# Kernel tuning notes

Hardware: AMD Instinct MI355X
Metric: run time of the kernel (lower is better)

Reference implementation:

```python
import jax, jax.numpy as jnp
import numpy as np

EMB = 1024
HID = 4096
B = 2
T = 4096
NUM_BLOCK = 24
EPS = 1e-6


def rmsnorm(x):
    # unparameterized RMS normalization over last dim
    return x * jax.lax.rsqrt(jnp.mean(jnp.square(x), axis=-1, keepdims=True) + EPS)


def setup_inputs() -> dict:
    key = jax.random.key(0)
    k1, k2, k3, k4 = jax.random.split(key, 4)
    x = jax.random.normal(k1, (B, T, EMB), dtype=jnp.float32)
    W1 = 0.02 * jax.random.normal(k2, (HID, EMB), dtype=jnp.float32)
    W2 = 0.02 * jax.random.normal(k3, (HID, EMB), dtype=jnp.float32)
    W3 = (0.02 / np.sqrt(NUM_BLOCK)) * jax.random.normal(k4, (EMB, HID), dtype=jnp.float32)
    return {"x": x, "W1": W1, "W2": W2, "W3": W3}


def bar_quadratic_causal_preact_stable(a, b):
    # y_t = (1/t^2) * sum_{i<=t} sum_{j<=t} exp(a_i + b_j), per feature channel.
    # exp factorizes, so compute stably via log-cumsum-exp along the seq axis.
    seq = a.shape[1]
    log_t = jnp.log(jnp.arange(1, seq + 1, dtype=a.dtype))  # [T]
    la = jax.lax.cumlogsumexp(a, axis=1)  # [B,T,H]
    lb = jax.lax.cumlogsumexp(b, axis=1)  # [B,T,H]
    return jnp.exp(la + lb - 2.0 * log_t[None, :, None])


def reference(x, W1, W2, W3):
    r = rmsnorm(x)
    a = jnp.einsum('bte,he->bth', r, W1)  # fc_1, no bias
    b = jnp.einsum('bte,he->bth', r, W2)  # fc_2, no bias
    r = bar_quadratic_causal_preact_stable(a, b)
    r = rmsnorm(r)
    r = jnp.einsum('bth,eh->bte', r, W3)  # fc_3, no bias
    return x + r
```

## Files before the change

### kernel.cpp

```cpp
#include <hip/hip_runtime.h>
#include <hip/hip_fp8.h>

#define EMB 1024
#define HID 4096
#define NB 2
#define TT 4096
#define MROWS (NB*TT)
#define N1 (2*HID)
#define CHUNK 128
#define NCH 32

typedef short short8 __attribute__((ext_vector_type(8)));
typedef float v4f   __attribute__((ext_vector_type(4)));

__device__ __forceinline__ unsigned short f2bf(float f) {
  unsigned int u = __float_as_uint(f);
  u += 0x7FFFu + ((u >> 16) & 1u);
  return (unsigned short)(u >> 16);
}
__device__ __forceinline__ float bf2f(unsigned short s) {
  return __uint_as_float(((unsigned int)s) << 16);
}
__device__ __forceinline__ float h2f(unsigned short u) {
  return (float)(*(const _Float16*)&u);
}
__device__ __forceinline__ unsigned char f2e4m3(float f) {
  __hip_fp8_e4m3 q(f);
  return *(unsigned char*)&q;
}
__device__ __forceinline__ float e4m32f(unsigned char c) {
  __hip_fp8_e4m3 q = *(__hip_fp8_e4m3*)&c;
  return (float)q;
}
__device__ __forceinline__ void g2l16(const void* g, void* l) {
  __builtin_amdgcn_global_load_lds(
      (const __attribute__((address_space(1))) void*)g,
      (__attribute__((address_space(3))) void*)l, 16, 0, 0);
}

__device__ __forceinline__ float block_reduce_sum(float v, float* sbuf) {
  #pragma unroll
  for (int off = 32; off; off >>= 1) v += __shfl_down(v, off, 64);
  int lane = threadIdx.x & 63, w = threadIdx.x >> 6;
  if (lane == 0) sbuf[w] = v;
  __syncthreads();
  return sbuf[0] + sbuf[1] + sbuf[2] + sbuf[3];
}

__global__ __launch_bounds__(256) void conv_all(const float* __restrict__ W1,
                                                const float* __restrict__ W2,
                                                const float* __restrict__ W3,
                                                unsigned short* __restrict__ o12,
                                                unsigned char* __restrict__ o3) {
  size_t i = ((size_t)blockIdx.x*256 + threadIdx.x)*4;
  if (i < 2ull*HID*EMB) {
    const float* s = (i < (size_t)HID*EMB) ? (W1 + i) : (W2 + (i - (size_t)HID*EMB));
    float4 v = *(const float4*)s;
    ushort4 u; u.x=f2bf(v.x); u.y=f2bf(v.y); u.z=f2bf(v.z); u.w=f2bf(v.w);
    *(ushort4*)(o12 + i) = u;
  } else {
    size_t off = i - 2ull*HID*EMB;
    float4 v = *(const float4*)(W3 + off);
    uchar4 u; u.x=f2e4m3(v.x*64.f); u.y=f2e4m3(v.y*64.f);
             u.z=f2e4m3(v.z*64.f); u.w=f2e4m3(v.w*64.f);
    *(uchar4*)(o3 + off) = u;
  }
}

__global__ __launch_bounds__(256) void rmsnorm_x(const float* __restrict__ x,
                                                 unsigned short* __restrict__ r) {
  __shared__ float sbuf[4];
  int row = blockIdx.x;
  float4 v = *(const float4*)(x + (size_t)row*EMB + threadIdx.x*4);
  float ss = v.x*v.x + v.y*v.y + v.z*v.z + v.w*v.w;
  float tot = block_reduce_sum(ss, sbuf);
  float sc = rsqrtf(tot * (1.0f/EMB) + 1e-6f);
  ushort4 o; o.x=f2bf(v.x*sc); o.y=f2bf(v.y*sc); o.z=f2bf(v.z*sc); o.w=f2bf(v.w*sc);
  *(ushort4*)(r + (size_t)row*EMB + threadIdx.x*4) = o;
}

__global__ __launch_bounds__(256) void normq(const unsigned short* __restrict__ y,
                                             unsigned char* __restrict__ y8) {
  __shared__ float sbuf[4];
  int row = blockIdx.x;
  const unsigned short* p = y + (size_t)row*HID + threadIdx.x*16;
  short8 v0 = *(const short8*)p;
  short8 v1 = *(const short8*)(p+8);
  float f[16]; float ss = 0.f;
  #pragma unroll
  for (int j=0;j<8;++j){ f[j]=bf2f((unsigned short)v0[j]); f[j+8]=bf2f((unsigned short)v1[j]); }
  #pragma unroll
  for (int j=0;j<16;++j) ss += f[j]*f[j];
  float tot = block_reduce_sum(ss, sbuf);
  float sc = rsqrtf(tot*(1.0f/HID) + 1e-6f);
  unsigned int w[4];
  #pragma unroll
  for (int g=0; g<4; ++g) {
    unsigned int a0 = f2e4m3(f[g*4+0]*sc);
    unsigned int a1 = f2e4m3(f[g*4+1]*sc);
    unsigned int a2 = f2e4m3(f[g*4+2]*sc);
    unsigned int a3 = f2e4m3(f[g*4+3]*sc);
    w[g] = a0 | (a1<<8) | (a2<<16) | (a3<<24);
  }
  uint4 o; o.x=w[0]; o.y=w[1]; o.z=w[2]; o.w=w[3];
  *(uint4*)(y8 + (size_t)row*HID + threadIdx.x*16) = o;
}

__global__ __launch_bounds__(512, 2)
void gemm_exp(const unsigned short* __restrict__ A,
              const unsigned short* __restrict__ Bt,
              unsigned char* __restrict__ C8,
              float* __restrict__ part,
              int K, int N) {
  __shared__ short lds[4][2][256*32];
  const int tid  = threadIdx.x;
  const int lane = tid & 63;
  const int wid  = tid >> 6;
  const int wr   = wid >> 2;
  const int wc   = wid & 3;
  const int bid  = blockIdx.x;
  const int s0   = bid >> 3;
  const int colTile = ((bid & 7) << 2) | (s0 & 3);
  const int rowTile = s0 >> 2;
  const int rowBase = rowTile << 8;
  const int colBase = colTile << 8;
  const int NT = K >> 5;

  v4f acc[8][4];
  #pragma unroll
  for (int i=0;i<8;++i)
    #pragma unroll
    for (int j=0;j<4;++j) acc[i][j] = (v4f){0.f,0.f,0.f,0.f};

  auto stage = [&](int t) {
    const int buf = t & 3;
    const int k0  = t << 5;
    #pragma unroll
    for (int j = 0; j < 2; ++j) {
      int slot = j*512 + tid;
      int msw  = slot >> 2;
      int m    = msw ^ ((msw >> 2) & 1);
      int c    = (slot & 3) ^ (m & 3);
      g2l16(A + (size_t)(rowBase + m)*K + k0 + c*8, &lds[buf][0][slot*8]);
    }
    #pragma unroll
    for (int j = 0; j < 2; ++j) {
      int slot = j*512 + tid;
      int msw  = slot >> 2;
      int m    = msw ^ ((msw >> 2) & 1);
      int c    = (slot & 3) ^ (m & 3);
      g2l16(Bt + (size_t)(colBase + m)*K + k0 + c*8, &lds[buf][1][slot*8]);
    }
  };

  stage(0);
  if (NT > 1) stage(1);

  const int q   = lane >> 4;
  const int r15 = lane & 15;

  for (int t = 0; t < NT; ++t) {
    if (t + 2 < NT) stage(t + 2);
    if (t + 2 < NT)      asm volatile("s_waitcnt vmcnt(8)" ::: "memory");
    else if (t + 1 < NT) asm volatile("s_waitcnt vmcnt(4)" ::: "memory");
    else                 asm volatile("s_waitcnt vmcnt(0)" ::: "memory");
    __builtin_amdgcn_s_barrier();
    __builtin_amdgcn_sched_barrier(0);

    const short* lA = &lds[t & 3][0][0];
    const short* lB = &lds[t & 3][1][0];
    short8 aF[4], bF[4], aG[4];
    #pragma unroll
    for (int mt = 0; mt < 4; ++mt) {
      int m = wr*128 + mt*16 + r15;
      int slot = ((m ^ ((m >> 2) & 1)) << 2) | (q ^ (m & 3));
      aF[mt] = *(const short8*)&lA[slot*8];
    }
    #pragma unroll
    for (int nt = 0; nt < 4; ++nt) {
      int n = wc*64 + nt*16 + r15;
      int slot = ((n ^ ((n >> 2) & 1)) << 2) | (q ^ (n & 3));
      bF[nt] = *(const short8*)&lB[slot*8];
    }
    #pragma unroll
    for (int mt = 0; mt < 4; ++mt) {
      int m = wr*128 + (mt+4)*16 + r15;
      int slot = ((m ^ ((m >> 2) & 1)) << 2) | (q ^ (m & 3));
      aG[mt] = *(const short8*)&lA[slot*8];
    }
    __builtin_amdgcn_s_setprio(1);
    #pragma unroll
    for (int mt = 0; mt < 4; ++mt)
      #pragma unroll
      for (int nt = 0; nt < 4; ++nt)
        acc[mt][nt] = __builtin_amdgcn_mfma_f32_16x16x32_bf16(aF[mt], bF[nt], acc[mt][nt], 0, 0, 0);
    #pragma unroll
    for (int mt = 0; mt < 4; ++mt)
      #pragma unroll
      for (int nt = 0; nt < 4; ++nt)
        acc[mt+4][nt] = __builtin_amdgcn_mfma_f32_16x16x32_bf16(aG[mt], bF[nt], acc[mt+4][nt], 0, 0, 0);
    __builtin_amdgcn_s_setprio(0);
  }

  float csum[4] = {0.f, 0.f, 0.f, 0.f};
  #pragma unroll
  for (int mt = 0; mt < 8; ++mt) {
    #pragma unroll
    for (int nt = 0; nt < 4; ++nt) {
      int col = colBase + wc*64 + nt*16 + r15;
      #pragma unroll
      for (int rr = 0; rr < 4; ++rr) {
        int row = rowBase + wr*128 + mt*16 + q*4 + rr;
        float e = __expf(acc[mt][nt][rr]);
        C8[(size_t)row*N + col] = f2e4m3(e);
        csum[nt] += e;
      }
    }
  }
  const int chunk = rowTile*2 + wr;
  #pragma unroll
  for (int nt = 0; nt < 4; ++nt) {
    float v = csum[nt];
    v += __shfl_xor(v, 16, 64);
    v += __shfl_xor(v, 32, 64);
    if (lane < 16)
      part[(size_t)(colBase + wc*64 + nt*16 + lane)*64 + chunk] = v;
  }
}

__global__ __launch_bounds__(256, 2)
void gemm_out(const unsigned char* __restrict__ A8,
              const unsigned char* __restrict__ B8,
              unsigned short* __restrict__ Ph,
              int K, int KCH, int N) {
  __shared__ unsigned char lA8[128*128];
  __shared__ unsigned char lB8[128*128];
  const int tid  = threadIdx.x;
  const int lane = tid & 63;
  const int wm   = (tid >> 6) >> 1, wn = (tid >> 6) & 1;
  const int rowBase = blockIdx.x * 128;
  const int colBase = blockIdx.y * 128;
  const int kStart  = blockIdx.z * KCH;

  v4f acc[4][4];
  #pragma unroll
  for (int i=0;i<4;++i)
    #pragma unroll
    for (int j=0;j<4;++j) acc[i][j] = (v4f){0.f,0.f,0.f,0.f};

  for (int k0 = kStart; k0 < kStart + KCH; k0 += 128) {
    #pragma unroll
    for (int j = 0; j < 4; ++j) {
      int s = j*256 + tid;
      int m = s >> 3;
      int c = (s & 7) ^ (m & 7);
      g2l16(A8 + (size_t)(rowBase + m)*K + k0 + c*16, &lA8[s*16]);
    }
    #pragma unroll
    for (int j = 0; j < 4; ++j) {
      int s = j*256 + tid;
      int m = s >> 3;
      int c = (s & 7) ^ (m & 7);
      g2l16(B8 + (size_t)(colBase + m)*K + k0 + c*16, &lB8[s*16]);
    }
    __syncthreads();
    #pragma unroll
    for (int s2 = 0; s2 < 4; ++s2) {
      const int quad = lane >> 4;
      const int cc = s2*2 + (quad >> 1);
      const int hh = quad & 1;
      long aF[4], bF[4];
      #pragma unroll
      for (int mt = 0; mt < 4; ++mt) {
        int ml = wm*64 + mt*16 + (lane & 15);
        aF[mt] = *(const long*)&lA8[ml*128 + ((cc ^ (ml & 7))<<4) + (hh<<3)];
      }
      #pragma unroll
      for (int nt = 0; nt < 4; ++nt) {
        int nl = wn*64 + nt*16 + (lane & 15);
        bF[nt] = *(const long*)&lB8[nl*128 + ((cc ^ (nl & 7))<<4) + (hh<<3)];
      }
      #pragma unroll
      for (int mt = 0; mt < 4; ++mt)
        #pragma unroll
        for (int nt = 0; nt < 4; ++nt)
          acc[mt][nt] = __builtin_amdgcn_mfma_f32_16x16x32_fp8_fp8(aF[mt], bF[nt], acc[mt][nt], 0, 0, 0);
    }
    __syncthreads();
  }

  const int quad = lane >> 4, c15 = lane & 15;
  #pragma unroll
  for (int mt = 0; mt < 4; ++mt) {
    #pragma unroll
    for (int nt = 0; nt < 4; ++nt) {
      int col = colBase + wn*64 + nt*16 + c15;
      #pragma unroll
      for (int r = 0; r < 4; ++r) {
        int row = rowBase + wm*64 + mt*16 + quad*4 + r;
        size_t idx = ((size_t)blockIdx.z*MROWS + row)*N + col;
        _Float16 h = (_Float16)acc[mt][nt][r];
        Ph[idx] = *(unsigned short*)&h;
      }
    }
  }
}

__global__ __launch_bounds__(256) void scan_prefix(float* __restrict__ part) {
  int idx = blockIdx.x*256 + threadIdx.x;
  int col = idx >> 1, bb = idx & 1;
  float* p = part + (size_t)col*64 + bb*NCH;
  float run = 0.f;
  #pragma unroll
  for (int c = 0; c < NCH; ++c) { float v = p[c]; p[c] = run; run += v; }
}

__global__ __launch_bounds__(256) void scan_emit(const unsigned char* __restrict__ ab,
                                                 const float* __restrict__ part,
                                                 unsigned short* __restrict__ y) {
  int h = blockIdx.x*256 + threadIdx.x;
  int cy = blockIdx.y, bb = blockIdx.z;
  float sa = part[(size_t)h*64 + bb*NCH + cy];
  float sb = part[(size_t)(HID + h)*64 + bb*NCH + cy];
  const unsigned char* pa = ab + ((size_t)(bb*TT + cy*CHUNK))*N1 + h;
  const unsigned char* pb = pa + HID;
  unsigned short* py = y + ((size_t)(bb*TT + cy*CHUNK))*HID + h;
  int t0 = cy*CHUNK;
  #pragma unroll 4
  for (int i = 0; i < CHUNK; ++i) {
    sa += e4m32f(pa[(size_t)i*N1]);
    sb += e4m32f(pb[(size_t)i*N1]);
    float inv = 1.0f / (float)(t0 + i + 1);
    py[(size_t)i*HID] = f2bf(sa*sb*inv*inv);
  }
}

__global__ __launch_bounds__(256) void reduce_out(const unsigned short* __restrict__ p,
                                                  const float* __restrict__ x,
                                                  float* __restrict__ o) {
  size_t i = ((size_t)blockIdx.x*256 + threadIdx.x)*4;
  float4 xv = *(const float4*)(x + i);
  float s0 = 0.f, s1 = 0.f, s2 = 0.f, s3 = 0.f;
  #pragma unroll
  for (int z = 0; z < 4; ++z) {
    ushort4 u = *(const ushort4*)(p + (size_t)z*MROWS*EMB + i);
    s0 += h2f(u.x); s1 += h2f(u.y); s2 += h2f(u.z); s3 += h2f(u.w);
  }
  const float inv64 = 1.0f/64.0f;
  float4 ov; ov.x = xv.x + inv64*s0; ov.y = xv.y + inv64*s1;
             ov.z = xv.z + inv64*s2; ov.w = xv.w + inv64*s3;
  *(float4*)(o + i) = ov;
}

extern "C" void kernel_launch(void* const* d_in, const int* in_sizes, int n_in,
                              void* d_out, int out_size, void* d_ws, size_t ws_size,
                              hipStream_t stream) {
  const float* x  = (const float*)d_in[0];
  const float* W1 = (const float*)d_in[1];
  const float* W2 = (const float*)d_in[2];
  const float* W3 = (const float*)d_in[3];
  float* out = (float*)d_out;
  char* ws = (char*)d_ws;

  unsigned short* r_bf   = (unsigned short*)(ws);
  unsigned short* w12_bf = (unsigned short*)(ws + 16777216ull);
  unsigned char*  w3_8   = (unsigned char*) (ws + 33554432ull);
  unsigned char*  ab8    = (unsigned char*) (ws + 37748736ull);
  unsigned short* y_bf   = (unsigned short*)(ws + 104857600ull);
  unsigned char*  y8     = (unsigned char*) (ws + 171966464ull);
  unsigned short* psum   = (unsigned short*)ab8;
  float*          part   = (float*)d_out;

  conv_all<<<12288, 256, 0, stream>>>(W1, W2, W3, w12_bf, w3_8);
  rmsnorm_x<<<MROWS, 256, 0, stream>>>(x, r_bf);
  gemm_exp<<<1024, 512, 0, stream>>>(r_bf, w12_bf, ab8, part, EMB, N1);
  scan_prefix<<<64, 256, 0, stream>>>(part);
  scan_emit<<<dim3(16,NCH,2), 256, 0, stream>>>(ab8, part, y_bf);
  normq<<<MROWS, 256, 0, stream>>>(y_bf, y8);
  gemm_out<<<dim3(64,8,4), 256, 0, stream>>>(y8, w3_8, psum, HID, 1024, EMB);
  reduce_out<<<8192, 256, 0, stream>>>(psum, x, out);
}
```

Baseline: 384.4 us.

## Restructure gemm_exp mainloop into four-phase ping-pong with interleaved half-tile staging

```diff
diff --git a/kernel.cpp b/kernel.cpp
--- a/kernel.cpp
+++ b/kernel.cpp
@@ -112,7 +112,8 @@
               unsigned char* __restrict__ C8,
               float* __restrict__ part,
               int K, int N) {
-  __shared__ short lds[4][2][256*32];
+  __shared__ short sA[2][2][8192];
+  __shared__ short sB[2][2][8192];
   const int tid  = threadIdx.x;
   const int lane = tid & 63;
   const int wid  = tid >> 6;
@@ -124,82 +125,128 @@
   const int rowTile = s0 >> 2;
   const int rowBase = rowTile << 8;
   const int colBase = colTile << 8;
-  const int NT = K >> 5;
-
-  v4f acc[8][4];
-  #pragma unroll
-  for (int i=0;i<8;++i)
-    #pragma unroll
-    for (int j=0;j<4;++j) acc[i][j] = (v4f){0.f,0.f,0.f,0.f};
-
-  auto stage = [&](int t) {
-    const int buf = t & 3;
-    const int k0  = t << 5;
-    #pragma unroll
-    for (int j = 0; j < 2; ++j) {
-      int slot = j*512 + tid;
-      int msw  = slot >> 2;
-      int m    = msw ^ ((msw >> 2) & 1);
-      int c    = (slot & 3) ^ (m & 3);
-      g2l16(A + (size_t)(rowBase + m)*K + k0 + c*8, &lds[buf][0][slot*8]);
-    }
-    #pragma unroll
-    for (int j = 0; j < 2; ++j) {
-      int slot = j*512 + tid;
-      int msw  = slot >> 2;
-      int m    = msw ^ ((msw >> 2) & 1);
-      int c    = (slot & 3) ^ (m & 3);
-      g2l16(Bt + (size_t)(colBase + m)*K + k0 + c*8, &lds[buf][1][slot*8]);
-    }
-  };
-
-  stage(0);
-  if (NT > 1) stage(1);
-
+  const int NT = K >> 6;
   const int q   = lane >> 4;
   const int r15 = lane & 15;
 
+  v4f acc[8][4];
+  #pragma unroll
+  for (int i=0;i<8;++i)
+    #pragma unroll
+    for (int j=0;j<4;++j) acc[i][j] = (v4f){0.f,0.f,0.f,0.f};
+
+  auto stageA = [&](int T, int kh) {
+    int Tw = (T >= NT) ? T - NT : T;
+    int kb = (Tw << 6) + (kh << 5);
+    short* dst = &sA[T & 1][kh][0];
+    #pragma unroll
+    for (int j = 0; j < 2; ++j) {
+      int s = j*512 + tid;
+      int m = s >> 2;
+      int c = (s & 3) ^ ((m >> 1) & 3);
+      g2l16(A + (size_t)(rowBase + m)*K + kb + c*8, dst + s*8);
+    }
+  };
+  auto stageB = [&](int T, int kh) {
+    int Tw = (T >= NT) ? T - NT : T;
+    int kb = (Tw << 6) + (kh << 5);
+    short* dst = &sB[T & 1][kh][0];
+    #pragma unroll
+    for (int j = 0; j < 2; ++j) {
+      int s = j*512 + tid;
+      int m = s >> 2;
+      int c = (s & 3) ^ ((m >> 1) & 3);
+      g2l16(Bt + (size_t)(colBase + m)*K + kb + c*8, dst + s*8);
+    }
+  };
+  auto rdA = [&](int mt, int kh, int buf) -> short8 {
+    int m = wr*128 + mt*16 + r15;
+    int slot = m*4 + (q ^ ((m >> 1) & 3));
+    return *(const short8*)&sA[buf][kh][slot*8];
+  };
+  auto rdB = [&](int nt, int kh, int buf) -> short8 {
+    int n = wc*64 + nt*16 + r15;
+    int slot = n*4 + (q ^ ((n >> 1) & 3));
+    return *(const short8*)&sB[buf][kh][slot*8];
+  };
+
+  stageA(0, 0); stageB(0, 0); stageA(0, 1); stageB(0, 1); stageA(1, 0);
+  asm volatile("s_waitcnt vmcnt(6)" ::: "memory");
+  __builtin_amdgcn_s_barrier();
+
   for (int t = 0; t < NT; ++t) {
-    if (t + 2 < NT) stage(t + 2);
-    if (t + 2 < NT)      asm volatile("s_waitcnt vmcnt(8)" ::: "memory");
-    else if (t + 1 < NT) asm volatile("s_waitcnt vmcnt(4)" ::: "memory");
-    else                 asm volatile("s_waitcnt vmcnt(0)" ::: "memory");
-    __builtin_amdgcn_s_barrier();
-    __builtin_amdgcn_sched_barrier(0);
-
-    const short* lA = &lds[t & 3][0][0];
-    const short* lB = &lds[t & 3][1][0];
-    short8 aF[4], bF[4], aG[4];
-    #pragma unroll
-    for (int mt = 0; mt < 4; ++mt) {
-      int m = wr*128 + mt*16 + r15;
-      int slot = ((m ^ ((m >> 2) & 1)) << 2) | (q ^ (m & 3));
-      aF[mt] = *(const short8*)&lA[slot*8];
-    }
-    #pragma unroll
-    for (int nt = 0; nt < 4; ++nt) {
-      int n = wc*64 + nt*16 + r15;
-      int slot = ((n ^ ((n >> 2) & 1)) << 2) | (q ^ (n & 3));
-      bF[nt] = *(const short8*)&lB[slot*8];
-    }
-    #pragma unroll
-    for (int mt = 0; mt < 4; ++mt) {
-      int m = wr*128 + (mt+4)*16 + r15;
-      int slot = ((m ^ ((m >> 2) & 1)) << 2) | (q ^ (m & 3));
-      aG[mt] = *(const short8*)&lA[slot*8];
-    }
+    const int buf = t & 1;
+    short8 aFr[4], bK0[4], bK1[4];
+
+    #pragma unroll
+    for (int mt = 0; mt < 4; ++mt) aFr[mt] = rdA(mt, 0, buf);
+    #pragma unroll
+    for (int nt = 0; nt < 4; ++nt) bK0[nt] = rdB(nt, 0, buf);
+    stageB(t + 1, 0);
+    __builtin_amdgcn_sched_barrier(0);
+    __builtin_amdgcn_s_barrier();
+    asm volatile("s_waitcnt lgkmcnt(0)" ::: "memory");
+    __builtin_amdgcn_sched_barrier(0);
     __builtin_amdgcn_s_setprio(1);
     #pragma unroll
     for (int mt = 0; mt < 4; ++mt)
       #pragma unroll
       for (int nt = 0; nt < 4; ++nt)
-        acc[mt][nt] = __builtin_amdgcn_mfma_f32_16x16x32_bf16(aF[mt], bF[nt], acc[mt][nt], 0, 0, 0);
+        acc[mt][nt] = __builtin_amdgcn_mfma_f32_16x16x32_bf16(aFr[mt], bK0[nt], acc[mt][nt], 0, 0, 0);
+    __builtin_amdgcn_s_setprio(0);
+    asm volatile("s_waitcnt vmcnt(4)" ::: "memory");
+    __builtin_amdgcn_s_barrier();
+
+    #pragma unroll
+    for (int mt = 0; mt < 4; ++mt) aFr[mt] = rdA(mt, 1, buf);
+    #pragma unroll
+    for (int nt = 0; nt < 4; ++nt) bK1[nt] = rdB(nt, 1, buf);
+    stageA(t + 1, 1);
+    __builtin_amdgcn_sched_barrier(0);
+    __builtin_amdgcn_s_barrier();
+    asm volatile("s_waitcnt lgkmcnt(0)" ::: "memory");
+    __builtin_amdgcn_sched_barrier(0);
+    __builtin_amdgcn_s_setprio(1);
     #pragma unroll
     for (int mt = 0; mt < 4; ++mt)
       #pragma unroll
       for (int nt = 0; nt < 4; ++nt)
-        acc[mt+4][nt] = __builtin_amdgcn_mfma_f32_16x16x32_bf16(aG[mt], bF[nt], acc[mt+4][nt], 0, 0, 0);
+        acc[mt][nt] = __builtin_amdgcn_mfma_f32_16x16x32_bf16(aFr[mt], bK1[nt], acc[mt][nt], 0, 0, 0);
     __builtin_amdgcn_s_setprio(0);
+    __builtin_amdgcn_s_barrier();
+
+    #pragma unroll
+    for (int mt = 0; mt < 4; ++mt) aFr[mt] = rdA(mt + 4, 0, buf);
+    stageB(t + 1, 1);
+    __builtin_amdgcn_sched_barrier(0);
+    __builtin_amdgcn_s_barrier();
+    asm volatile("s_waitcnt lgkmcnt(0)" ::: "memory");
+    __builtin_amdgcn_sched_barrier(0);
+    __builtin_amdgcn_s_setprio(1);
+    #pragma unroll
+    for (int mt = 0; mt < 4; ++mt)
+      #pragma unroll
+      for (int nt = 0; nt < 4; ++nt)
+        acc[mt+4][nt] = __builtin_amdgcn_mfma_f32_16x16x32_bf16(aFr[mt], bK0[nt], acc[mt+4][nt], 0, 0, 0);
+    __builtin_amdgcn_s_setprio(0);
+    __builtin_amdgcn_s_barrier();
+
+    #pragma unroll
+    for (int mt = 0; mt < 4; ++mt) aFr[mt] = rdA(mt + 4, 1, buf);
+    stageA(t + 2, 0);
+    __builtin_amdgcn_sched_barrier(0);
+    __builtin_amdgcn_s_barrier();
+    asm volatile("s_waitcnt lgkmcnt(0)" ::: "memory");
+    __builtin_amdgcn_sched_barrier(0);
+    __builtin_amdgcn_s_setprio(1);
+    #pragma unroll
+    for (int mt = 0; mt < 4; ++mt)
+      #pragma unroll
+      for (int nt = 0; nt < 4; ++nt)
+        acc[mt+4][nt] = __builtin_amdgcn_mfma_f32_16x16x32_bf16(aFr[mt], bK1[nt], acc[mt+4][nt], 0, 0, 0);
+    __builtin_amdgcn_s_setprio(0);
+    asm volatile("s_waitcnt vmcnt(6)" ::: "memory");
+    __builtin_amdgcn_s_barrier();
   }
 
   float csum[4] = {0.f, 0.f, 0.f, 0.f};
```

New measurement: 382.8 us. About the same (-0.4%).
